# Performance work log

Measured on AMD Instinct MI355X. Metric: run time of the kernel, lower is better.

## Reference

```python
import jax, jax.numpy as jnp
import numpy as np


def setup_inputs() -> dict:
    key = jax.random.key(0)
    ks = jax.random.split(key, 20)
    B, N, C = 8, 16384, 3

    def w(k, shape, scale=0.1):
        return jax.random.normal(k, shape, dtype=jnp.float32) * scale

    inp = {
        "points": jax.random.normal(ks[0], (B, N, C), dtype=jnp.float32),
        # first_layer: Conv1d(3,64,k=1)+BN+ReLU  (BN folded to scale s, shift t)
        "w0": w(ks[1], (64, 3)), "b0": w(ks[2], (64,)),
        "s0": 1.0 + w(ks[3], (64,), 0.05), "t0": w(ks[4], (64,), 0.05),
        # mlp1[3:]: Conv1d(64,64,k=1)+BN+ReLU
        "w1": w(ks[5], (64, 64)), "b1": w(ks[6], (64,)),
        "s1": 1.0 + w(ks[7], (64,), 0.05), "t1": w(ks[8], (64,), 0.05),
        # mlp2: Conv1d(64,128)+BN+ReLU, Conv1d(128,1024)+BN+ReLU
        "w2": w(ks[9], (128, 64)), "b2": w(ks[10], (128,)),
        "s2": 1.0 + w(ks[11], (128,), 0.05), "t2": w(ks[12], (128,), 0.05),
        "w3": w(ks[13], (1024, 128)), "b3": w(ks[14], (1024,)),
        "s3": 1.0 + w(ks[15], (1024,), 0.05), "t3": w(ks[16], (1024,), 0.05),
        "M": 512,
        "R": 32,
    }
    return inp


def _block(h, w, b, s, t):
    # pointwise Conv1d (k=1) + eval-mode BatchNorm (folded affine) + ReLU
    y = jnp.einsum('bmri,oi->bmro', h, w) + b
    return jax.nn.relu(y * s + t)


def reference(points, w0, b0, s0, t0, w1, b1, s1, t1,
              w2, b2, s2, t2, w3, b3, s3, t3, M, R):
    B, N, C = points.shape
    xyz = points[..., :3]
    barange = jnp.arange(B)

    # --- sampling: iteratively pick point farthest from the LAST centroid
    # (faithful to the original, which uses only centroids[i], not min-dist FPS)
    def step(last, _):
        d = jnp.sqrt(jnp.sum((xyz - last[:, None, :3]) ** 2, axis=-1))  # [B,N]
        ind = jnp.argmax(d, axis=-1)                                    # [B]
        new = points[barange, ind]                                      # [B,C]
        return new, new

    first = points[:, 0]  # deterministic stand-in for the random initial index
    _, rest = jax.lax.scan(step, first, None, length=M - 1)
    centroids = jnp.concatenate(
        [first[:, None], jnp.swapaxes(rest, 0, 1)], axis=1)  # [B,M,C]

    # --- grouping: R nearest points to each centroid
    d = jnp.sqrt(jnp.sum(
        (xyz[:, None] - centroids[:, :, None, :3]) ** 2, axis=-1))  # [B,M,N]
    _, idx = jax.lax.top_k(-d, R)                                    # [B,M,R]
    groups = points[barange[:, None, None], idx]                     # [B,M,R,C]

    # --- pointnet: shared pointwise MLP + max over group, vectorized over M
    h = _block(groups, w0, b0, s0, t0)   # [B,M,R,64]
    h = _block(h, w1, b1, s1, t1)        # [B,M,R,64]
    h = _block(h, w2, b2, s2, t2)        # [B,M,R,128]
    h = _block(h, w3, b3, s3, t3)        # [B,M,R,1024]
    g = jnp.max(h, axis=2)               # [B,M,1024]
    return g[..., None]                  # [B,M,1024,1]
```

## Files before the change

### kernel.cpp

```cpp
#include <hip/hip_runtime.h>

#define NPT 16384
#define MC  512
#define BATCH 8
#define CAP 512
#define LCAP 128

typedef __attribute__((ext_vector_type(8))) __bf16 bf16x8;
typedef __attribute__((ext_vector_type(4))) float f32x4;
typedef __attribute__((ext_vector_type(16))) float f32x16;

static __device__ __forceinline__ unsigned short f2bf(float f) {
    unsigned int u = __float_as_uint(f);
    unsigned int r = (u + 0x7FFFu + ((u >> 16) & 1u)) >> 16;
    return (unsigned short)r;
}

static __device__ __forceinline__ float dist2(float x, float y, float z,
                                              float cx, float cy, float cz) {
    float dx = x - cx, dy = y - cy, dz = z - cz;
    return __fadd_rn(__fadd_rn(__fmul_rn(dx, dx), __fmul_rn(dy, dy)), __fmul_rn(dz, dz));
}

__global__ void prep_all(const float* __restrict__ points,
                         const float* __restrict__ w1, const float* __restrict__ b1,
                         const float* __restrict__ s1, const float* __restrict__ t1,
                         const float* __restrict__ w2, const float* __restrict__ b2,
                         const float* __restrict__ s2, const float* __restrict__ t2,
                         const float* __restrict__ w3, const float* __restrict__ b3,
                         const float* __restrict__ s3, const float* __restrict__ t3,
                         unsigned short* __restrict__ Wp1, unsigned short* __restrict__ Wp2,
                         unsigned short* __restrict__ Wp3,
                         float* __restrict__ bias1, float* __restrict__ bias2,
                         float* __restrict__ bias3, float4* __restrict__ pts4,
                         int* __restrict__ gcnt) {
    int i = blockIdx.x * blockDim.x + threadIdx.x;
    if (i < 64 * 64) {
        int o = i >> 6;
        Wp1[i] = f2bf(w1[i] * s1[o]);
    } else if (i < 64 * 64 + 128 * 64) {
        int j = i - 4096; int o = j >> 6;
        Wp2[j] = f2bf(w2[j] * s2[o]);
    } else if (i < 64 * 64 + 128 * 64 + 1024 * 128) {
        int j = i - 12288; int o = j >> 7; int col = j & 127;
        int scol = (((col >> 3) ^ (o & 7)) << 3) | (col & 7);
        Wp3[j] = f2bf(w3[(o << 7) | scol] * s3[o]);
    }
    if (i < 64)   bias1[i] = b1[i] * s1[i] + t1[i];
    if (i < 128)  bias2[i] = b2[i] * s2[i] + t2[i];
    if (i < 1024) bias3[i] = b3[i] * s3[i] + t3[i];
    if (i < BATCH * MC) gcnt[i] = 0;
    if (i < BATCH * NPT) {
        const float* p = points + (size_t)i * 3;
        float x = p[0], y = p[1], z = p[2];
        pts4[i] = make_float4(x, y, z, x * x + y * y + z * z);
    }
}

__global__ __launch_bounds__(1024) void fps_kernel(const float* __restrict__ pts,
                                                   float* __restrict__ cent) {
    int b = blockIdx.x;
    const float* P = pts + (size_t)b * NPT * 3;
    float* C = cent + (size_t)b * MC * 3;
    __shared__ int hist[MC];
    __shared__ float curx, cury, curz;
    __shared__ float rd[16];
    __shared__ int ri[16];
    __shared__ int s_found, s_j;

    int tid = threadIdx.x;
    int i0 = tid * 16;
    float px[16], py[16], pz[16];
#pragma unroll
    for (int j = 0; j < 16; j++) {
        px[j] = P[(i0 + j) * 3 + 0];
        py[j] = P[(i0 + j) * 3 + 1];
        pz[j] = P[(i0 + j) * 3 + 2];
    }
    if (tid == 0) {
        hist[0] = 0;
        curx = P[0]; cury = P[1]; curz = P[2];
        C[0] = P[0]; C[1] = P[1]; C[2] = P[2];
        s_found = 0; s_j = 0;
    }
    __syncthreads();

    int t;
    for (t = 1; t < MC; t++) {
        float cx = curx, cy = cury, cz = curz;
        float bd = -1.0f; int bi = 0;
#pragma unroll
        for (int j = 0; j < 16; j++) {
            float dx = px[j] - cx, dy = py[j] - cy, dz = pz[j] - cz;
            float d2 = __fadd_rn(__fadd_rn(__fmul_rn(dx, dx), __fmul_rn(dy, dy)), __fmul_rn(dz, dz));
            float d = __fsqrt_rn(d2);
            if (d > bd) { bd = d; bi = i0 + j; }
        }
#pragma unroll
        for (int off = 32; off; off >>= 1) {
            float od = __shfl_xor(bd, off);
            int   oi = __shfl_xor(bi, off);
            if (od > bd || (od == bd && oi < bi)) { bd = od; bi = oi; }
        }
        int wid = tid >> 6;
        if ((tid & 63) == 0) { rd[wid] = bd; ri[wid] = bi; }
        __syncthreads();
        if (tid == 0) {
            float fb = rd[0]; int fi = ri[0];
            for (int wv = 1; wv < 16; wv++)
                if (rd[wv] > fb || (rd[wv] == fb && ri[wv] < fi)) { fb = rd[wv]; fi = ri[wv]; }
            int found = -1;
            for (int j = 0; j < t; j++) if (hist[j] == fi) { found = j; break; }
            hist[t] = fi;
            s_j = found;
            curx = P[fi * 3]; cury = P[fi * 3 + 1]; curz = P[fi * 3 + 2];
            C[t * 3] = curx; C[t * 3 + 1] = cury; C[t * 3 + 2] = curz;
            s_found = (found >= 0);
        }
        __syncthreads();
        if (s_found) break;
    }
    if (s_found && t < MC - 1) {
        int j = s_j, p = t - s_j;
        for (int k = t + 1 + tid; k < MC; k += 1024) {
            int src = j + (k - j) % p;
            int ind = hist[src];
            C[k * 3] = P[ind * 3]; C[k * 3 + 1] = P[ind * 3 + 1]; C[k * 3 + 2] = P[ind * 3 + 2];
        }
    }
}

__global__ __launch_bounds__(256) void bound_gather_kernel(
    const float4* __restrict__ pts4, const float* __restrict__ cent,
    int* __restrict__ gcnt, unsigned long long* __restrict__ gcand) {
    int tid = threadIdx.x, wv = tid >> 6, lane = tid & 63;
    int blk = blockIdx.x;
    int grp = blk >> 2;
    int chunk = blk & 3;
    int b = grp >> 6;
    int gbase = grp * 8;
    const float4* P4 = pts4 + (size_t)b * NPT + chunk * 4096;

    __shared__ float smin[8][256];
    __shared__ float sB[8];
    __shared__ int lcnt[8];
    __shared__ unsigned long long lcand[8][LCAP];
    __shared__ int gslot[8];

    if (tid < 8) lcnt[tid] = 0;

    float cx[8], cy[8], cz[8], hc[8];
#pragma unroll
    for (int c = 0; c < 8; c++) {
        cx[c] = __uint_as_float(__builtin_amdgcn_readfirstlane(__float_as_uint(cent[(size_t)(gbase + c) * 3 + 0])));
        cy[c] = __uint_as_float(__builtin_amdgcn_readfirstlane(__float_as_uint(cent[(size_t)(gbase + c) * 3 + 1])));
        cz[c] = __uint_as_float(__builtin_amdgcn_readfirstlane(__float_as_uint(cent[(size_t)(gbase + c) * 3 + 2])));
        hc[c] = cx[c] * cx[c] + cy[c] * cy[c] + cz[c] * cz[c];
    }

    float lmin[8];
#pragma unroll
    for (int c = 0; c < 8; c++) lmin[c] = 3.4e38f;
#pragma unroll 4
    for (int k = 0; k < 16; k++) {
        float4 p = P4[tid + k * 256];
#pragma unroll
        for (int c = 0; c < 8; c++) {
            float t = fmaf(p.x, cx[c], fmaf(p.y, cy[c], p.z * cz[c]));
            float d2 = fmaxf(fmaf(-2.0f, t, p.w + hc[c]), 0.0f);
            lmin[c] = fminf(lmin[c], d2);
        }
    }
#pragma unroll
    for (int c = 0; c < 8; c++) smin[c][tid] = lmin[c];
    __syncthreads();

    for (int cc = 0; cc < 2; ++cc) {
        int c = wv * 2 + cc;
        float4 q = *(const float4*)&smin[c][lane << 2];
        float m = fminf(fminf(q.x, q.y), fminf(q.z, q.w));
        unsigned int mb = __float_as_uint(m);
        unsigned int T = 0;
#pragma unroll
        for (int bit = 30; bit >= 0; --bit) {
            unsigned int cnd = T | (1u << bit);
            int cnt = __popcll(__ballot(mb < cnd));
            if (cnt <= 31) T = cnd;
        }
        if (lane == 0) sB[c] = __uint_as_float(T);
    }
    __syncthreads();
    float Bf[8];
#pragma unroll
    for (int c = 0; c < 8; c++) Bf[c] = sB[c];

#pragma unroll 4
    for (int k = 0; k < 16; k++) {
        int il = tid + k * 256;
        float4 p = P4[il];
        unsigned int gi = (unsigned int)(chunk * 4096 + il);
#pragma unroll
        for (int c = 0; c < 8; c++) {
            float s = p.w + hc[c];
            float t = fmaf(p.x, cx[c], fmaf(p.y, cy[c], p.z * cz[c]));
            float d2f = fmaf(-2.0f, t, s);
            float eps = fmaf(8e-7f, s, 4e-6f);
            if (d2f - eps <= Bf[c]) {
                int pslot = atomicAdd(&lcnt[c], 1);
                if (pslot < LCAP) {
                    float d2x = dist2(p.x, p.y, p.z, cx[c], cy[c], cz[c]);
                    unsigned int sb = __float_as_uint(__fsqrt_rn(d2x));
                    lcand[c][pslot] = ((unsigned long long)sb << 32) | gi;
                }
            }
        }
    }
    __syncthreads();

    if (tid < 8) {
        int c = tid, n = lcnt[c];
        int add = (n > LCAP) ? 1000000 : n;
        gslot[c] = atomicAdd(&gcnt[gbase + c], add);
    }
    __syncthreads();
    for (int cc = 0; cc < 2; ++cc) {
        int c = wv * 2 + cc;
        int n = lcnt[c] < LCAP ? lcnt[c] : LCAP;
        int base = gslot[c];
        for (int q = lane; q < n; q += 64) {
            int pos = base + q;
            if (pos < CAP) gcand[(size_t)(gbase + c) * CAP + pos] = lcand[c][q];
        }
    }
}

__global__ __launch_bounds__(256) void select_l0_kernel(
    const float4* __restrict__ pts4, const float* __restrict__ cent,
    const int* __restrict__ gcnt, const unsigned long long* __restrict__ gcand,
    const float* __restrict__ w0, const float* __restrict__ b0,
    const float* __restrict__ s0, const float* __restrict__ t0,
    unsigned short* __restrict__ h0) {
    int tid = threadIdx.x, wv = tid >> 6, lane = tid & 63;
    int g = blockIdx.x * 4 + wv;
    int b = g >> 9;
    const float4* P4 = pts4 + (size_t)b * NPT;

    __shared__ unsigned long long scand[4][CAP];
    __shared__ float sxyz[4][32][3];

    int n = gcnt[g];
    int nc = n < CAP ? n : CAP;
    for (int q = lane; q < nc; q += 64) scand[wv][q] = gcand[(size_t)g * CAP + q];

    unsigned long long sel = 0, last = 0;
    if (n <= CAP) {
        for (int s = 0; s < 32; s++) {
            unsigned long long best = ~0ull;
            for (int q = lane; q < nc; q += 64) {
                unsigned long long kk = scand[wv][q];
                if ((s == 0 || kk > last) && kk < best) best = kk;
            }
#pragma unroll
            for (int off = 32; off; off >>= 1) {
                unsigned long long o = __shfl_xor(best, off);
                best = o < best ? o : best;
            }
            last = best;
            if (lane == s) sel = best;
        }
    } else {
        for (int s = 0; s < 32; s++) {
            unsigned long long best = ~0ull;
            float ccx = cent[(size_t)g * 3], ccy = cent[(size_t)g * 3 + 1], ccz = cent[(size_t)g * 3 + 2];
            for (int i = lane; i < NPT; i += 64) {
                float4 p = P4[i];
                float d2 = dist2(p.x, p.y, p.z, ccx, ccy, ccz);
                unsigned int db = __float_as_uint(__fsqrt_rn(d2));
                unsigned long long kk = ((unsigned long long)db << 32) | (unsigned int)i;
                if ((s == 0 || kk > last) && kk < best) best = kk;
            }
#pragma unroll
            for (int off = 32; off; off >>= 1) {
                unsigned long long o = __shfl_xor(best, off);
                best = o < best ? o : best;
            }
            last = best;
            if (lane == s) sel = best;
        }
    }
    if (lane < 32) {
        unsigned int idx = (unsigned int)sel;
        if (idx >= NPT) idx = 0;
        float4 p = P4[idx];
        sxyz[wv][lane][0] = p.x;
        sxyz[wv][lane][1] = p.y;
        sxyz[wv][lane][2] = p.z;
    }

    int o = lane;
    float sw = s0[o];
    float fw0 = w0[o * 3] * sw, fw1 = w0[o * 3 + 1] * sw, fw2 = w0[o * 3 + 2] * sw;
    float fb = b0[o] * sw + t0[o];
    size_t base = ((size_t)g * 32) * 64 + o;
#pragma unroll 8
    for (int r = 0; r < 32; r++) {
        float x = sxyz[wv][r][0], y = sxyz[wv][r][1], z = sxyz[wv][r][2];
        float acc = fmaf(z, fw2, fmaf(y, fw1, fmaf(x, fw0, fb)));
        h0[base + (size_t)r * 64] = f2bf(fmaxf(acc, 0.0f));
    }
}

template <int N>
__global__ __launch_bounds__(256) void gemm_relu_kernel(
    const unsigned short* __restrict__ A, const unsigned short* __restrict__ W,
    const float* __restrict__ bias, unsigned short* __restrict__ Out) {
    __shared__ unsigned short sW[N * 64];
    int tid = threadIdx.x, w = tid >> 6, lane = tid & 63, lr = lane & 15, lq = lane >> 4;
    const int SWEEPS = (N * 64 * 2) / 4096;
#pragma unroll
    for (int sweep = 0; sweep < SWEEPS; ++sweep) {
        int r = sweep * 32 + (tid >> 3), s = tid & 7;
        int ss = s ^ (r & 7);
        *(uint4*)&sW[r * 64 + s * 8] = *(const uint4*)&W[r * 64 + ss * 8];
    }
    __syncthreads();

    int row0 = blockIdx.x * 256 + w * 64;
    const int NT = N / 16;
    f32x4 acc[4][NT];
#pragma unroll
    for (int m = 0; m < 4; m++)
#pragma unroll
        for (int n = 0; n < NT; n++) acc[m][n] = (f32x4){0.f, 0.f, 0.f, 0.f};

    bf16x8 a[4][2];
#pragma unroll
    for (int m = 0; m < 4; m++)
#pragma unroll
        for (int ks = 0; ks < 2; ks++)
            a[m][ks] = *(const bf16x8*)&A[(size_t)(row0 + m * 16 + lr) * 64 + ks * 32 + lq * 8];

#pragma unroll
    for (int ks = 0; ks < 2; ks++)
#pragma unroll
        for (int n = 0; n < NT; n++) {
            bf16x8 wf = *(const bf16x8*)&sW[(n * 16 + lr) * 64 + (((ks * 4 + lq) ^ (lr & 7)) * 8)];
#pragma unroll
            for (int m = 0; m < 4; m++)
                acc[m][n] = __builtin_amdgcn_mfma_f32_16x16x32_bf16(a[m][ks], wf, acc[m][n], 0, 0, 0);
        }

#pragma unroll
    for (int n = 0; n < NT; n++) {
        int col = n * 16 + lr;
        float bb = bias[col];
#pragma unroll
        for (int m = 0; m < 4; m++)
#pragma unroll
            for (int i = 0; i < 4; i++) {
                int rr = row0 + m * 16 + lq * 4 + i;
                Out[(size_t)rr * N + col] = f2bf(fmaxf(acc[m][n][i] + bb, 0.f));
            }
    }
}

__global__ __launch_bounds__(256) void gemm3_max_kernel(
    const unsigned short* __restrict__ A, const unsigned short* __restrict__ W,
    const float* __restrict__ bias, float* __restrict__ Out) {
    __shared__ unsigned short sW[128 * 128];
    int tid = threadIdx.x, w = tid >> 6, lane = tid & 63;
    int l32 = lane & 31, hi = lane >> 5;
    int wr = w >> 1, wc = w & 1;
    int row0 = blockIdx.x * 128 + wr * 64;
    int g0 = row0 >> 5;

    bf16x8 a[2][8];
#pragma unroll
    for (int m = 0; m < 2; m++)
#pragma unroll
        for (int ks = 0; ks < 8; ks++)
            a[m][ks] = *(const bf16x8*)&A[(size_t)(row0 + m * 32 + l32) * 128 + ks * 16 + hi * 8];

    for (int cb = 0; cb < 8; ++cb) {
#pragma unroll
        for (int j = 0; j < 8; ++j) {
            const unsigned short* g = W + (size_t)cb * 16384 + w * 4096 + j * 512 + lane * 8;
            __builtin_amdgcn_global_load_lds(
                (const __attribute__((address_space(1))) void*)g,
                (__attribute__((address_space(3))) void*)&sW[w * 4096 + j * 512],
                16, 0, 0);
        }
        __syncthreads();

        f32x16 acc[2][2];
#pragma unroll
        for (int m = 0; m < 2; m++)
#pragma unroll
            for (int n = 0; n < 2; n++)
#pragma unroll
                for (int r = 0; r < 16; r++) acc[m][n][r] = 0.f;

#pragma unroll
        for (int ks = 0; ks < 8; ks++)
#pragma unroll
            for (int n = 0; n < 2; n++) {
                int rw = wc * 64 + n * 32 + l32;
                int slot = (ks * 2 + hi) ^ (rw & 7);
                bf16x8 wf = *(const bf16x8*)&sW[rw * 128 + slot * 8];
#pragma unroll
                for (int m = 0; m < 2; m++)
                    acc[m][n] = __builtin_amdgcn_mfma_f32_32x32x16_bf16(a[m][ks], wf, acc[m][n], 0, 0, 0);
            }

#pragma unroll
        for (int n = 0; n < 2; n++) {
            int col = cb * 128 + wc * 64 + n * 32 + l32;
            float bb = bias[col];
#pragma unroll
            for (int m = 0; m < 2; m++) {
                float t0_ = fmaxf(acc[m][n][0], acc[m][n][1]);
                float t1_ = fmaxf(acc[m][n][2], acc[m][n][3]);
                float t2_ = fmaxf(acc[m][n][4], acc[m][n][5]);
                float t3_ = fmaxf(acc[m][n][6], acc[m][n][7]);
                float t4_ = fmaxf(acc[m][n][8], acc[m][n][9]);
                float t5_ = fmaxf(acc[m][n][10], acc[m][n][11]);
                float t6_ = fmaxf(acc[m][n][12], acc[m][n][13]);
                float t7_ = fmaxf(acc[m][n][14], acc[m][n][15]);
                float u0 = fmaxf(t0_, t1_), u1 = fmaxf(t2_, t3_);
                float u2 = fmaxf(t4_, t5_), u3 = fmaxf(t6_, t7_);
                float v = fmaxf(fmaxf(u0, u1), fmaxf(u2, u3));
                v = fmaxf(v, __shfl_xor(v, 32));
                v = fmaxf(v + bb, 0.f);
                if (hi == 0) Out[(size_t)(g0 + m) * 1024 + col] = v;
            }
        }
        __syncthreads();
    }
}

extern "C" void kernel_launch(void* const* d_in, const int* in_sizes, int n_in,
                              void* d_out, int out_size, void* d_ws, size_t ws_size,
                              hipStream_t stream) {
    const float* points = (const float*)d_in[0];
    const float* w0 = (const float*)d_in[1];
    const float* b0 = (const float*)d_in[2];
    const float* s0 = (const float*)d_in[3];
    const float* t0 = (const float*)d_in[4];
    const float* w1 = (const float*)d_in[5];
    const float* b1 = (const float*)d_in[6];
    const float* s1 = (const float*)d_in[7];
    const float* t1 = (const float*)d_in[8];
    const float* w2 = (const float*)d_in[9];
    const float* b2 = (const float*)d_in[10];
    const float* s2 = (const float*)d_in[11];
    const float* t2 = (const float*)d_in[12];
    const float* w3 = (const float*)d_in[13];
    const float* b3 = (const float*)d_in[14];
    const float* s3 = (const float*)d_in[15];
    const float* t3 = (const float*)d_in[16];

    char* ws = (char*)d_ws;
    float* cent = (float*)(ws + 0);
    unsigned short* Wp1 = (unsigned short*)(ws + 49152);
    unsigned short* Wp2 = (unsigned short*)(ws + 57344);
    unsigned short* Wp3 = (unsigned short*)(ws + 73728);
    float* bias1 = (float*)(ws + 335872);
    float* bias2 = (float*)(ws + 336128);
    float* bias3 = (float*)(ws + 336640);
    unsigned short* h0 = (unsigned short*)(ws + 340736);
    unsigned short* h1 = (unsigned short*)(ws + 340736 + 16777216);
    unsigned short* h2 = (unsigned short*)(ws + 340736 + 2 * 16777216);
    int* gcnt = (int*)(ws + 340736 + 3 * 16777216);
    float4* pts4 = (float4*)h2;
    unsigned long long* gcand = (unsigned long long*)h1;
    float* out = (float*)d_out;

    hipLaunchKernelGGL(prep_all, dim3(560), dim3(256), 0, stream,
                       points, w1, b1, s1, t1, w2, b2, s2, t2, w3, b3, s3, t3,
                       Wp1, Wp2, Wp3, bias1, bias2, bias3, pts4, gcnt);
    hipLaunchKernelGGL(fps_kernel, dim3(BATCH), dim3(1024), 0, stream, points, cent);
    hipLaunchKernelGGL(bound_gather_kernel, dim3(2048), dim3(256), 0, stream,
                       pts4, cent, gcnt, gcand);
    hipLaunchKernelGGL(select_l0_kernel, dim3(1024), dim3(256), 0, stream,
                       pts4, cent, gcnt, gcand, w0, b0, s0, t0, h0);
    hipLaunchKernelGGL((gemm_relu_kernel<64>), dim3(512), dim3(256), 0, stream, h0, Wp1, bias1, h1);
    hipLaunchKernelGGL((gemm_relu_kernel<128>), dim3(512), dim3(256), 0, stream, h1, Wp2, bias2, h2);
    hipLaunchKernelGGL(gemm3_max_kernel, dim3(1024), dim3(256), 0, stream, h2, Wp3, bias3, out);
}
```

Baseline: 174.0 us.

## Use exact distances and 16 centroids per block in candidate gather

```diff
diff --git a/kernel.cpp b/kernel.cpp
--- a/kernel.cpp
+++ b/kernel.cpp
@@ -4,7 +4,7 @@
 #define MC  512
 #define BATCH 8
 #define CAP 512
-#define LCAP 128
+#define LCAP 96
 
 typedef __attribute__((ext_vector_type(8))) __bf16 bf16x8;
 typedef __attribute__((ext_vector_type(4))) float f32x4;
@@ -52,8 +52,7 @@
     if (i < BATCH * MC) gcnt[i] = 0;
     if (i < BATCH * NPT) {
         const float* p = points + (size_t)i * 3;
-        float x = p[0], y = p[1], z = p[2];
-        pts4[i] = make_float4(x, y, z, x * x + y * y + z * z);
+        pts4[i] = make_float4(p[0], p[1], p[2], 0.0f);
     }
 }
 
@@ -135,48 +134,44 @@
     int* __restrict__ gcnt, unsigned long long* __restrict__ gcand) {
     int tid = threadIdx.x, wv = tid >> 6, lane = tid & 63;
     int blk = blockIdx.x;
-    int grp = blk >> 2;
-    int chunk = blk & 3;
-    int b = grp >> 6;
-    int gbase = grp * 8;
-    const float4* P4 = pts4 + (size_t)b * NPT + chunk * 4096;
-
-    __shared__ float smin[8][256];
-    __shared__ float sB[8];
-    __shared__ int lcnt[8];
-    __shared__ unsigned long long lcand[8][LCAP];
-    __shared__ int gslot[8];
-
-    if (tid < 8) lcnt[tid] = 0;
-
-    float cx[8], cy[8], cz[8], hc[8];
-#pragma unroll
-    for (int c = 0; c < 8; c++) {
+    int grp = blk >> 3;
+    int chunk = blk & 7;
+    int b = grp >> 5;
+    int gbase = grp * 16;
+    const float4* P4 = pts4 + (size_t)b * NPT + chunk * 2048;
+
+    __shared__ float smin[16][256];
+    __shared__ unsigned int sU[16];
+    __shared__ int lcnt[16];
+    __shared__ unsigned long long lcand[16][LCAP];
+    __shared__ int gslot[16];
+
+    if (tid < 16) lcnt[tid] = 0;
+
+    float cx[16], cy[16], cz[16];
+#pragma unroll
+    for (int c = 0; c < 16; c++) {
         cx[c] = __uint_as_float(__builtin_amdgcn_readfirstlane(__float_as_uint(cent[(size_t)(gbase + c) * 3 + 0])));
         cy[c] = __uint_as_float(__builtin_amdgcn_readfirstlane(__float_as_uint(cent[(size_t)(gbase + c) * 3 + 1])));
         cz[c] = __uint_as_float(__builtin_amdgcn_readfirstlane(__float_as_uint(cent[(size_t)(gbase + c) * 3 + 2])));
-        hc[c] = cx[c] * cx[c] + cy[c] * cy[c] + cz[c] * cz[c];
-    }
-
-    float lmin[8];
-#pragma unroll
-    for (int c = 0; c < 8; c++) lmin[c] = 3.4e38f;
-#pragma unroll 4
-    for (int k = 0; k < 16; k++) {
+    }
+
+    float lmin[16];
+#pragma unroll
+    for (int c = 0; c < 16; c++) lmin[c] = 3.4e38f;
+#pragma unroll 2
+    for (int k = 0; k < 8; k++) {
         float4 p = P4[tid + k * 256];
 #pragma unroll
-        for (int c = 0; c < 8; c++) {
-            float t = fmaf(p.x, cx[c], fmaf(p.y, cy[c], p.z * cz[c]));
-            float d2 = fmaxf(fmaf(-2.0f, t, p.w + hc[c]), 0.0f);
-            lmin[c] = fminf(lmin[c], d2);
-        }
-    }
-#pragma unroll
-    for (int c = 0; c < 8; c++) smin[c][tid] = lmin[c];
-    __syncthreads();
-
-    for (int cc = 0; cc < 2; ++cc) {
-        int c = wv * 2 + cc;
+        for (int c = 0; c < 16; c++)
+            lmin[c] = fminf(lmin[c], dist2(p.x, p.y, p.z, cx[c], cy[c], cz[c]));
+    }
+#pragma unroll
+    for (int c = 0; c < 16; c++) smin[c][tid] = lmin[c];
+    __syncthreads();
+
+    for (int cc = 0; cc < 4; ++cc) {
+        int c = wv * 4 + cc;
         float4 q = *(const float4*)&smin[c][lane << 2];
         float m = fminf(fminf(q.x, q.y), fminf(q.z, q.w));
         unsigned int mb = __float_as_uint(m);
@@ -187,29 +182,28 @@
             int cnt = __popcll(__ballot(mb < cnd));
             if (cnt <= 31) T = cnd;
         }
-        if (lane == 0) sB[c] = __uint_as_float(T);
-    }
-    __syncthreads();
-    float Bf[8];
-#pragma unroll
-    for (int c = 0; c < 8; c++) Bf[c] = sB[c];
-
-#pragma unroll 4
-    for (int k = 0; k < 16; k++) {
+        float s = __fsqrt_rn(__uint_as_float(T));
+        unsigned int u = T;
+        for (int it = 0; it < 8 && __fsqrt_rn(__uint_as_float(u + 1u)) <= s; ++it) u++;
+        if (lane == 0) sU[c] = u;
+    }
+    __syncthreads();
+    unsigned int U[16];
+#pragma unroll
+    for (int c = 0; c < 16; c++) U[c] = sU[c];
+
+#pragma unroll 2
+    for (int k = 0; k < 8; k++) {
         int il = tid + k * 256;
         float4 p = P4[il];
-        unsigned int gi = (unsigned int)(chunk * 4096 + il);
-#pragma unroll
-        for (int c = 0; c < 8; c++) {
-            float s = p.w + hc[c];
-            float t = fmaf(p.x, cx[c], fmaf(p.y, cy[c], p.z * cz[c]));
-            float d2f = fmaf(-2.0f, t, s);
-            float eps = fmaf(8e-7f, s, 4e-6f);
-            if (d2f - eps <= Bf[c]) {
+        unsigned int gi = (unsigned int)(chunk * 2048 + il);
+#pragma unroll
+        for (int c = 0; c < 16; c++) {
+            float d2 = dist2(p.x, p.y, p.z, cx[c], cy[c], cz[c]);
+            if (__float_as_uint(d2) <= U[c]) {
                 int pslot = atomicAdd(&lcnt[c], 1);
                 if (pslot < LCAP) {
-                    float d2x = dist2(p.x, p.y, p.z, cx[c], cy[c], cz[c]);
-                    unsigned int sb = __float_as_uint(__fsqrt_rn(d2x));
+                    unsigned int sb = __float_as_uint(__fsqrt_rn(d2));
                     lcand[c][pslot] = ((unsigned long long)sb << 32) | gi;
                 }
             }
@@ -217,14 +211,14 @@
     }
     __syncthreads();
 
-    if (tid < 8) {
+    if (tid < 16) {
         int c = tid, n = lcnt[c];
         int add = (n > LCAP) ? 1000000 : n;
         gslot[c] = atomicAdd(&gcnt[gbase + c], add);
     }
     __syncthreads();
-    for (int cc = 0; cc < 2; ++cc) {
-        int c = wv * 2 + cc;
+    for (int cc = 0; cc < 4; ++cc) {
+        int c = wv * 4 + cc;
         int n = lcnt[c] < LCAP ? lcnt[c] : LCAP;
         int base = gslot[c];
         for (int q = lane; q < n; q += 64) {
```

Result: slower. 189.4 us (+8.8%).
